# Kernel optimization log

Measured on AMD Instinct MI355X. Metric: run time of the kernel, lower is better.

## Reference

```python
import jax, jax.numpy as jnp
import numpy as np

B, C, H, W = 8, 64, 256, 256   # input images
FH, FW = 64, 64                # low-res feature map
S = 256                        # superpixels per image (num[i] == S)


def setup_inputs() -> dict:
    key = jax.random.key(0)
    k1, k2, k3 = jax.random.split(key, 3)
    inp = jax.random.normal(k1, (B, C, H, W), dtype=jnp.float32)
    feat = jax.random.normal(k2, (B, C, FH, FW), dtype=jnp.float32)
    sp = jax.random.randint(k3, (B, 1, H, W), 0, S).astype(jnp.int64)
    num = jnp.full((B,), S, dtype=jnp.int64)
    return {"input": inp, "feature": feat, "sp": sp, "num": num}


def bilinear_align_corners(x, out_h, out_w):
    # F.interpolate(x, size, mode='bilinear', align_corners=True)
    _, _, in_h, in_w = x.shape
    ys = jnp.linspace(0.0, in_h - 1.0, out_h)
    xs = jnp.linspace(0.0, in_w - 1.0, out_w)
    y0 = jnp.floor(ys).astype(jnp.int32)
    x0 = jnp.floor(xs).astype(jnp.int32)
    y1 = jnp.minimum(y0 + 1, in_h - 1)
    x1 = jnp.minimum(x0 + 1, in_w - 1)
    wy = (ys - y0.astype(ys.dtype)).reshape(1, 1, out_h, 1)
    wx = (xs - x0.astype(xs.dtype)).reshape(1, 1, 1, out_w)
    rows = x[:, :, y0, :] * (1.0 - wy) + x[:, :, y1, :] * wy   # [B,C,out_h,in_w]
    return rows[:, :, :, x0] * (1.0 - wx) + rows[:, :, :, x1] * wx


def segment_scalar_means(x, sp, num):
    # torch: mean_values[i][j] = mean(x[i][sp[i]==j]) over channels AND pixels
    b = x.shape[0]
    px = x.mean(axis=1).reshape(b, -1)           # channel-mean per pixel [B, HW]
    ids = sp.reshape(b, -1)                      # [B, HW]
    seg_sum = jax.vmap(lambda v, i: jax.ops.segment_sum(v, i, num_segments=S))(px, ids)
    seg_cnt = jax.vmap(lambda i: jax.ops.segment_sum(jnp.ones(i.shape, jnp.float32), i, num_segments=S))(ids)
    m = jnp.where(seg_cnt > 0, seg_sum / jnp.maximum(seg_cnt, 1.0), 0.0)  # nan_to_num(0)
    valid = jnp.arange(S)[None, :] < num[:, None]                          # j < num[i]
    return jnp.where(valid, m, 0.0)              # [B, S]


def similarity_matrix(m):
    # mean_values broadcast to [B,S,C] => 1 - ||diff||/sqrt(C) == 1 - |m_j - m_k|
    return 1.0 - jnp.abs(m[:, :, None] - m[:, None, :])   # [B, S, S]


def reference(input, feature, sp, num):
    feat = bilinear_align_corners(feature, input.shape[-1], input.shape[-1])
    mat1 = similarity_matrix(segment_scalar_means(input, sp, num))
    mat2 = similarity_matrix(segment_scalar_means(feat, sp, num))
    return jnp.mean(jnp.abs(mat1 - mat2))   # nn.L1Loss()
```

## Files before the change

### kernel.cpp

```cpp
#include <hip/hip_runtime.h>

#define NB 8
#define NC 64
#define NH 256
#define NW 256
#define HW (NH*NW)
#define NFH 64
#define NFW 64
#define FHW (NFH*NFW)
#define NS 256
#define PPB 1024
#define BLKS_PER_IMG (HW / PPB)

__global__ void fmean_zero_k(const float* __restrict__ feature,
                             float* __restrict__ fmean,
                             float* __restrict__ sum1,
                             float* __restrict__ sum2,
                             unsigned* __restrict__ cnt) {
  if (blockIdx.x < 128) {
    int idx = blockIdx.x * 256 + threadIdx.x;
    int b  = idx >> 12;
    int fp = idx & 4095;
    const float* src = feature + (size_t)b * NC * FHW + fp;
    float a = 0.f;
    #pragma unroll
    for (int c = 0; c < NC; ++c) a += src[(size_t)c * FHW];
    fmean[idx] = a * (1.0f / NC);
  } else {
    for (int i = threadIdx.x; i < NB * NS; i += 256) {
      sum1[i] = 0.f; sum2[i] = 0.f; cnt[i] = 0u;
    }
  }
}

__global__ __launch_bounds__(256) void
main_k(const float* __restrict__ input,
       const int* __restrict__ sp,
       const float* __restrict__ fmean,
       float* __restrict__ sum1,
       float* __restrict__ sum2,
       unsigned* __restrict__ cnt) {
  __shared__ float s_f[FHW];
  __shared__ float s_sum1[NS];
  __shared__ float s_sum2[NS];
  __shared__ unsigned s_cnt[NS];

  const int b     = blockIdx.x >> 6;
  const int pbase = (blockIdx.x & (BLKS_PER_IMG - 1)) * PPB;
  const int tid   = threadIdx.x;

  const float* fsrc = fmean + (size_t)b * FHW;
  for (int i = tid; i < FHW; i += 256) s_f[i] = fsrc[i];
  s_sum1[tid] = 0.f; s_sum2[tid] = 0.f; s_cnt[tid] = 0u;
  __syncthreads();

  const int p0 = pbase + tid * 4;
  const float* ibase = input + (size_t)b * NC * HW + p0;

  float4 acc = make_float4(0.f, 0.f, 0.f, 0.f);
  #pragma unroll 8
  for (int c = 0; c < NC; ++c) {
    float4 v = *reinterpret_cast<const float4*>(ibase + (size_t)c * HW);
    acc.x += v.x; acc.y += v.y; acc.z += v.z; acc.w += v.w;
  }
  const float inv_c = 1.0f / NC;
  float px[4] = {acc.x * inv_c, acc.y * inv_c, acc.z * inv_c, acc.w * inv_c};

  int4 idv = *reinterpret_cast<const int4*>(sp + (size_t)b * HW + p0);
  int ids[4] = {idv.x, idv.y, idv.z, idv.w};

  #pragma unroll
  for (int i = 0; i < 4; ++i) {
    const int p = p0 + i;
    const int h = p >> 8;
    const int w = p & 255;
    double yd = (double)(h * (NFH - 1)) / (double)(NH - 1);
    double xd = (double)(w * (NFW - 1)) / (double)(NW - 1);
    int y0 = (int)yd;
    int x0 = (int)xd;
    float wy = (float)(yd - (double)y0);
    float wx = (float)(xd - (double)x0);
    int y1 = min(y0 + 1, NFH - 1);
    int x1 = min(x0 + 1, NFW - 1);
    float f00 = s_f[y0 * NFW + x0], f01 = s_f[y0 * NFW + x1];
    float f10 = s_f[y1 * NFW + x0], f11 = s_f[y1 * NFW + x1];
    float fv = (f00 * (1.f - wx) + f01 * wx) * (1.f - wy)
             + (f10 * (1.f - wx) + f11 * wx) * wy;

    atomicAdd(&s_sum1[ids[i]], px[i]);
    atomicAdd(&s_sum2[ids[i]], fv);
    atomicAdd(&s_cnt[ids[i]], 1u);
  }
  __syncthreads();

  atomicAdd(&sum1[b * NS + tid], s_sum1[tid]);
  atomicAdd(&sum2[b * NS + tid], s_sum2[tid]);
  atomicAdd(&cnt[b * NS + tid], s_cnt[tid]);
}

__global__ void finalize_k(const float* __restrict__ sum1,
                           const float* __restrict__ sum2,
                           const unsigned* __restrict__ cnt,
                           const int* __restrict__ num,
                           float* __restrict__ partial) {
  __shared__ float m1[NS];
  __shared__ float m2[NS];
  __shared__ float red[256];
  const int b = blockIdx.x;
  const int j = threadIdx.x;

  unsigned c = cnt[b * NS + j];
  int nb = num[b];
  float v1 = 0.f, v2 = 0.f;
  if (j < nb && c > 0u) {
    float invc = 1.0f / (float)c;
    v1 = sum1[b * NS + j] * invc;
    v2 = sum2[b * NS + j] * invc;
  }
  m1[j] = v1; m2[j] = v2;
  __syncthreads();

  const float a1 = v1, a2 = v2;
  float accum = 0.f;
  #pragma unroll 8
  for (int k = 0; k < NS; ++k) {
    accum += fabsf(fabsf(a1 - m1[k]) - fabsf(a2 - m2[k]));
  }
  red[j] = accum;
  __syncthreads();
  for (int s = 128; s > 0; s >>= 1) {
    if (j < s) red[j] += red[j + s];
    __syncthreads();
  }
  if (j == 0) partial[b] = red[0];
}

__global__ void final_k(const float* __restrict__ partial, float* __restrict__ out) {
  if (threadIdx.x == 0 && blockIdx.x == 0) {
    float s = 0.f;
    for (int b = 0; b < NB; ++b) s += partial[b];
    out[0] = s / (float)((long long)NB * NS * NS);
  }
}

extern "C" void kernel_launch(void* const* d_in, const int* in_sizes, int n_in,
                              void* d_out, int out_size, void* d_ws, size_t ws_size,
                              hipStream_t stream) {
  const float* input   = (const float*)d_in[0];
  const float* feature = (const float*)d_in[1];
  const int*   sp      = (const int*)d_in[2];
  const int*   num     = (const int*)d_in[3];
  float* out = (float*)d_out;

  float*    ws      = (float*)d_ws;
  float*    sum1    = ws;
  float*    sum2    = ws + 2048;
  unsigned* cnt     = (unsigned*)(ws + 4096);
  float*    partial = ws + 6144;
  float*    fmean   = ws + 8192;

  fmean_zero_k<<<129, 256, 0, stream>>>(feature, fmean, sum1, sum2, cnt);
  main_k<<<NB * BLKS_PER_IMG, 256, 0, stream>>>(input, sp, fmean, sum1, sum2, cnt);
  finalize_k<<<NB, 256, 0, stream>>>(sum1, sum2, cnt, num, partial);
  final_k<<<1, 64, 0, stream>>>(partial, out);
}
```

Baseline: 60.79 us.

## Split channel reduction across more blocks and replace global atomics with partial buffers

Work in the main kernel now splits by channel group: 2048 blocks each sum 16 channels of one pixel tile into a private histogram, and 512 separate blocks do the bilinear feature interpolation and counts. Per-block histograms go to partial buffers instead of global atomics, so the zero-init kernel is removed and the finalize kernel reduces 256 or 64 partials per image. Interpolation now uses float arithmetic instead of double, and the feature mean kernel is vectorised. The aim is more parallelism for the bandwidth-bound 134 MB input read and less atomic contention. In exchange there are more partial writes, a heavier serial reduction in a finalize kernel that runs only 8 blocks, and possible float rounding differences in the interpolation weights.

```diff
diff --git a/kernel.cpp b/kernel.cpp
--- a/kernel.cpp
+++ b/kernel.cpp
@@ -10,121 +10,150 @@
 #define FHW (NFH*NFW)
 #define NS 256
 #define PPB 1024
-#define BLKS_PER_IMG (HW / PPB)
+#define NPB (HW/PPB)
+#define NG 4
+#define CPG (NC/NG)
+#define NA (NB*NPB*NG)
+#define NBB (NB*NPB)
 
-__global__ void fmean_zero_k(const float* __restrict__ feature,
-                             float* __restrict__ fmean,
-                             float* __restrict__ sum1,
-                             float* __restrict__ sum2,
-                             unsigned* __restrict__ cnt) {
-  if (blockIdx.x < 128) {
-    int idx = blockIdx.x * 256 + threadIdx.x;
-    int b  = idx >> 12;
-    int fp = idx & 4095;
-    const float* src = feature + (size_t)b * NC * FHW + fp;
-    float a = 0.f;
-    #pragma unroll
-    for (int c = 0; c < NC; ++c) a += src[(size_t)c * FHW];
-    fmean[idx] = a * (1.0f / NC);
-  } else {
-    for (int i = threadIdx.x; i < NB * NS; i += 256) {
-      sum1[i] = 0.f; sum2[i] = 0.f; cnt[i] = 0u;
-    }
+__global__ __launch_bounds__(256) void fmean_k(const float* __restrict__ feature,
+                                               float* __restrict__ fmean) {
+  int idx = blockIdx.x * 256 + threadIdx.x;
+  int b = idx >> 10;
+  int q = idx & 1023;
+  const float4* src = reinterpret_cast<const float4*>(feature + (size_t)b * NC * FHW) + q;
+  float4 a = make_float4(0.f, 0.f, 0.f, 0.f);
+  #pragma unroll 16
+  for (int c = 0; c < NC; ++c) {
+    float4 v = src[(size_t)c * (FHW / 4)];
+    a.x += v.x; a.y += v.y; a.z += v.z; a.w += v.w;
   }
+  const float s = 1.0f / NC;
+  a.x *= s; a.y *= s; a.z *= s; a.w *= s;
+  reinterpret_cast<float4*>(fmean)[idx] = a;
 }
 
 __global__ __launch_bounds__(256) void
 main_k(const float* __restrict__ input,
        const int* __restrict__ sp,
        const float* __restrict__ fmean,
-       float* __restrict__ sum1,
-       float* __restrict__ sum2,
-       unsigned* __restrict__ cnt) {
+       float* __restrict__ part1,
+       float* __restrict__ part2,
+       float* __restrict__ partc) {
   __shared__ float s_f[FHW];
-  __shared__ float s_sum1[NS];
-  __shared__ float s_sum2[NS];
+  __shared__ float s_bins[NS];
   __shared__ unsigned s_cnt[NS];
 
-  const int b     = blockIdx.x >> 6;
-  const int pbase = (blockIdx.x & (BLKS_PER_IMG - 1)) * PPB;
-  const int tid   = threadIdx.x;
+  const int bid = blockIdx.x;
+  const int tid = threadIdx.x;
 
-  const float* fsrc = fmean + (size_t)b * FHW;
-  for (int i = tid; i < FHW; i += 256) s_f[i] = fsrc[i];
-  s_sum1[tid] = 0.f; s_sum2[tid] = 0.f; s_cnt[tid] = 0u;
-  __syncthreads();
+  if (bid < NA) {
+    const int g  = bid & (NG - 1);
+    const int pb = (bid >> 2) & (NPB - 1);
+    const int b  = bid >> 8;
 
-  const int p0 = pbase + tid * 4;
-  const float* ibase = input + (size_t)b * NC * HW + p0;
+    s_bins[tid] = 0.f;
+    __syncthreads();
 
-  float4 acc = make_float4(0.f, 0.f, 0.f, 0.f);
-  #pragma unroll 8
-  for (int c = 0; c < NC; ++c) {
-    float4 v = *reinterpret_cast<const float4*>(ibase + (size_t)c * HW);
-    acc.x += v.x; acc.y += v.y; acc.z += v.z; acc.w += v.w;
+    const int p0 = pb * PPB + tid * 4;
+    const float* ib = input + ((size_t)(b * NC + g * CPG)) * HW + p0;
+    float4 acc = make_float4(0.f, 0.f, 0.f, 0.f);
+    #pragma unroll
+    for (int c = 0; c < CPG; ++c) {
+      float4 v = *reinterpret_cast<const float4*>(ib + (size_t)c * HW);
+      acc.x += v.x; acc.y += v.y; acc.z += v.z; acc.w += v.w;
+    }
+    const float s = 1.0f / NC;
+    int4 idv = *reinterpret_cast<const int4*>(sp + (size_t)b * HW + p0);
+    atomicAdd(&s_bins[idv.x], acc.x * s);
+    atomicAdd(&s_bins[idv.y], acc.y * s);
+    atomicAdd(&s_bins[idv.z], acc.z * s);
+    atomicAdd(&s_bins[idv.w], acc.w * s);
+    __syncthreads();
+
+    part1[(size_t)bid * NS + tid] = s_bins[tid];
+  } else {
+    const int r  = bid - NA;
+    const int b  = r >> 6;
+    const int pb = r & (NPB - 1);
+
+    const float4* fsrc = reinterpret_cast<const float4*>(fmean + (size_t)b * FHW);
+    #pragma unroll
+    for (int i = 0; i < 4; ++i)
+      reinterpret_cast<float4*>(s_f)[tid + 256 * i] = fsrc[tid + 256 * i];
+    s_bins[tid] = 0.f;
+    s_cnt[tid] = 0u;
+    __syncthreads();
+
+    const int p0 = pb * PPB + tid * 4;
+    int4 idv = *reinterpret_cast<const int4*>(sp + (size_t)b * HW + p0);
+    int ids[4] = {idv.x, idv.y, idv.z, idv.w};
+
+    const int h = p0 >> 8;
+    const float yd = (float)h * (63.0f / 255.0f);
+    const int y0 = (int)yd;
+    const float wy = yd - (float)y0;
+    const int y1 = min(y0 + 1, NFH - 1);
+    const float* row0 = s_f + y0 * NFW;
+    const float* row1 = s_f + y1 * NFW;
+
+    #pragma unroll
+    for (int i = 0; i < 4; ++i) {
+      const int w = (p0 & 255) + i;
+      const float xd = (float)w * (63.0f / 255.0f);
+      const int x0 = (int)xd;
+      const float wx = xd - (float)x0;
+      const int x1 = min(x0 + 1, NFW - 1);
+      float top = row0[x0] * (1.f - wx) + row0[x1] * wx;
+      float bot = row1[x0] * (1.f - wx) + row1[x1] * wx;
+      float fv = top * (1.f - wy) + bot * wy;
+      atomicAdd(&s_bins[ids[i]], fv);
+      atomicAdd(&s_cnt[ids[i]], 1u);
+    }
+    __syncthreads();
+
+    part2[(size_t)r * NS + tid] = s_bins[tid];
+    partc[(size_t)r * NS + tid] = (float)s_cnt[tid];
   }
-  const float inv_c = 1.0f / NC;
-  float px[4] = {acc.x * inv_c, acc.y * inv_c, acc.z * inv_c, acc.w * inv_c};
-
-  int4 idv = *reinterpret_cast<const int4*>(sp + (size_t)b * HW + p0);
-  int ids[4] = {idv.x, idv.y, idv.z, idv.w};
-
-  #pragma unroll
-  for (int i = 0; i < 4; ++i) {
-    const int p = p0 + i;
-    const int h = p >> 8;
-    const int w = p & 255;
-    double yd = (double)(h * (NFH - 1)) / (double)(NH - 1);
-    double xd = (double)(w * (NFW - 1)) / (double)(NW - 1);
-    int y0 = (int)yd;
-    int x0 = (int)xd;
-    float wy = (float)(yd - (double)y0);
-    float wx = (float)(xd - (double)x0);
-    int y1 = min(y0 + 1, NFH - 1);
-    int x1 = min(x0 + 1, NFW - 1);
-    float f00 = s_f[y0 * NFW + x0], f01 = s_f[y0 * NFW + x1];
-    float f10 = s_f[y1 * NFW + x0], f11 = s_f[y1 * NFW + x1];
-    float fv = (f00 * (1.f - wx) + f01 * wx) * (1.f - wy)
-             + (f10 * (1.f - wx) + f11 * wx) * wy;
-
-    atomicAdd(&s_sum1[ids[i]], px[i]);
-    atomicAdd(&s_sum2[ids[i]], fv);
-    atomicAdd(&s_cnt[ids[i]], 1u);
-  }
-  __syncthreads();
-
-  atomicAdd(&sum1[b * NS + tid], s_sum1[tid]);
-  atomicAdd(&sum2[b * NS + tid], s_sum2[tid]);
-  atomicAdd(&cnt[b * NS + tid], s_cnt[tid]);
 }
 
-__global__ void finalize_k(const float* __restrict__ sum1,
-                           const float* __restrict__ sum2,
-                           const unsigned* __restrict__ cnt,
-                           const int* __restrict__ num,
-                           float* __restrict__ partial) {
+__global__ __launch_bounds__(256) void
+finalize_k(const float* __restrict__ part1,
+           const float* __restrict__ part2,
+           const float* __restrict__ partc,
+           const int* __restrict__ num,
+           float* __restrict__ partial) {
   __shared__ float m1[NS];
   __shared__ float m2[NS];
   __shared__ float red[256];
   const int b = blockIdx.x;
   const int j = threadIdx.x;
 
-  unsigned c = cnt[b * NS + j];
-  int nb = num[b];
+  float s1 = 0.f;
+  const float* p1 = part1 + (size_t)b * 256 * NS + j;
+  #pragma unroll 8
+  for (int t = 0; t < 256; ++t) s1 += p1[(size_t)t * NS];
+
+  float s2 = 0.f, c = 0.f;
+  const float* p2 = part2 + (size_t)b * 64 * NS + j;
+  const float* pc = partc + (size_t)b * 64 * NS + j;
+  #pragma unroll 8
+  for (int t = 0; t < 64; ++t) { s2 += p2[(size_t)t * NS]; c += pc[(size_t)t * NS]; }
+
+  const int nb = num[b];
   float v1 = 0.f, v2 = 0.f;
-  if (j < nb && c > 0u) {
-    float invc = 1.0f / (float)c;
-    v1 = sum1[b * NS + j] * invc;
-    v2 = sum2[b * NS + j] * invc;
+  if (j < nb && c > 0.f) {
+    float invc = 1.0f / c;
+    v1 = s1 * invc;
+    v2 = s2 * invc;
   }
   m1[j] = v1; m2[j] = v2;
   __syncthreads();
 
-  const float a1 = v1, a2 = v2;
   float accum = 0.f;
   #pragma unroll 8
   for (int k = 0; k < NS; ++k) {
-    accum += fabsf(fabsf(a1 - m1[k]) - fabsf(a2 - m2[k]));
+    accum += fabsf(fabsf(v1 - m1[k]) - fabsf(v2 - m2[k]));
   }
   red[j] = accum;
   __syncthreads();
@@ -152,15 +181,15 @@
   const int*   num     = (const int*)d_in[3];
   float* out = (float*)d_out;
 
-  float*    ws      = (float*)d_ws;
-  float*    sum1    = ws;
-  float*    sum2    = ws + 2048;
-  unsigned* cnt     = (unsigned*)(ws + 4096);
-  float*    partial = ws + 6144;
-  float*    fmean   = ws + 8192;
+  float* ws      = (float*)d_ws;
+  float* part1   = ws;
+  float* part2   = ws + (size_t)NA * NS;
+  float* partc   = part2 + (size_t)NBB * NS;
+  float* fmean   = partc + (size_t)NBB * NS;
+  float* partial = fmean + NB * FHW;
 
-  fmean_zero_k<<<129, 256, 0, stream>>>(feature, fmean, sum1, sum2, cnt);
-  main_k<<<NB * BLKS_PER_IMG, 256, 0, stream>>>(input, sp, fmean, sum1, sum2, cnt);
-  finalize_k<<<NB, 256, 0, stream>>>(sum1, sum2, cnt, num, partial);
+  fmean_k<<<32, 256, 0, stream>>>(feature, fmean);
+  main_k<<<NA + NBB, 256, 0, stream>>>(input, sp, fmean, part1, part2, partc);
+  finalize_k<<<NB, 256, 0, stream>>>(part1, part2, partc, num, partial);
   final_k<<<1, 64, 0, stream>>>(partial, out);
 }
```

New measurement: 56.66 us. -6.8%, faster.
